# Performance work log

Hardware: AMD Instinct MI355X
Metric: run time of the kernel (lower is better)

## Reference

```python
import jax, jax.numpy as jnp
import numpy as np

ALPHA = 0.5
GAMMA = 0.01
TOP_K = 5
B, T, C = 2048, 8192, 1  # C must be 1 for amp_loss's grouped conv1d to be valid


def _ashift_loss(inp, tgt):
    _, t_len, _ = inp.shape
    sm = jax.nn.softmax(inp - tgt, axis=1)                      # [B,T,C]
    return jnp.mean(jnp.sum(jnp.abs(1.0 / t_len - sm), axis=1, keepdims=True))


def _phase_loss(inp, tgt, top_k=TOP_K):
    inp_f = jnp.fft.rfft(inp, axis=1)                           # [B,Tf,C] complex
    tgt_f = jnp.fft.rfft(tgt, axis=1)
    b, tf_len, c = tgt_f.shape
    amp = jnp.abs(tgt_f).at[:, 0, :].set(0.0)                   # zero DC bin
    # top-k magnitudes along freq axis (per batch, per channel)
    _, idx = jax.lax.top_k(jnp.transpose(amp, (0, 2, 1)), top_k)  # [B,C,k]
    top = jnp.transpose(idx, (0, 2, 1))                         # [B,k,C]
    # boolean mask: True everywhere except top-k freq bins (per column)
    freqs = jnp.arange(tf_len)
    mask = ~jnp.any(freqs[None, :, None, None] == top[:, None, :, :], axis=2)  # [B,Tf,C]
    # replicate torch row-major boolean-mask flatten + view(B, Tf-k, C):
    flat = mask.reshape(b, tf_len * c)
    order = jnp.argsort(~flat, axis=1, stable=True)             # kept (True) positions first, in row-major order
    keep = order[:, : (tf_len - top_k) * c]                     # flat (t*C + c') positions
    non_top = (keep // c).reshape(b, tf_len - top_k, c)         # stored value is the freq index t
    dom = jnp.take_along_axis(tgt_f, top, axis=1) - jnp.take_along_axis(inp_f, top, axis=1)
    domain_loss = jnp.mean(jnp.sqrt(jnp.sum(jnp.abs(dom) ** 2, axis=1)))
    gath = jnp.take_along_axis(inp_f, non_top, axis=1)          # [B,Tf-k,C]
    nondomain_loss = jnp.mean(jnp.sqrt(jnp.sum(jnp.abs(gath) ** 2, axis=1, keepdims=True)))
    return domain_loss + nondomain_loss


def _amp_loss(inp, tgt):
    # Valid only for C==1: conv1d([B,1,T], weight=[B,1,T], groups=1) -> [B,B,1]
    # out[b,o] = sum_t tgt[b,t] * flip(kernel)[o,t]
    t2 = tgt[:, :, 0]                                           # [B,T]
    i2 = inp[:, :, 0]
    flip_diff = t2[:, ::-1] - i2[:, ::-1]                       # flip(target) - flip(input)
    diff = jnp.einsum('bt,ot->bo', t2, flip_diff)               # self_corr - cross_corr, [B,B]
    # torch.norm(p=2) over the singleton dim == abs
    return jnp.mean(jnp.abs(diff))


def setup_inputs() -> dict:
    key = jax.random.key(0)
    k1, k2 = jax.random.split(key)
    inp = jax.random.normal(k1, (B, T, C), dtype=jnp.float32)
    tgt = jax.random.normal(k2, (B, T, C), dtype=jnp.float32)
    return {"input": inp, "target": tgt}


def reference(input, target):
    return (ALPHA * _ashift_loss(input, target)
            + (1.0 - ALPHA) * _phase_loss(input, target)
            + GAMMA * _amp_loss(input, target))
```

## Files before the change

### kernel.cpp

```cpp
#include <hip/hip_runtime.h>
#include <hip/hip_bf16.h>
#include <math.h>

#define B_N 2048
#define T_N 8192
#define NFFT 4096
#define TF_LEN 4097
#define TOPK 5
#define KSPLIT 4
#define GBK 64

#define ZIDX(n) ((n) + ((n) >> 4))
#define ZPAD (NFFT + (NFFT >> 4))

typedef float f32x4 __attribute__((ext_vector_type(4)));
typedef __bf16 bf16x8 __attribute__((ext_vector_type(8)));
typedef unsigned short ushort_t;

__device__ __forceinline__ void gload_lds16(const ushort_t* g, ushort_t* l) {
    __builtin_amdgcn_global_load_lds(
        (const __attribute__((address_space(1))) void*)g,
        (__attribute__((address_space(3))) void*)l,
        16, 0, 0);
}

__device__ __forceinline__ float wave_reduce_sum(float v) {
    for (int o = 32; o >= 1; o >>= 1) v += __shfl_xor(v, o, 64);
    return v;
}
__device__ __forceinline__ float wave_reduce_max(float v) {
    for (int o = 32; o >= 1; o >>= 1) v = fmaxf(v, __shfl_xor(v, o, 64));
    return v;
}

__device__ __forceinline__ ushort_t f2bf(float x) {
    __hip_bfloat16 h = __float2bfloat16(x);
    return *reinterpret_cast<ushort_t*>(&h);
}

__device__ __forceinline__ float2 cis_rev(float rev) {
    return make_float2(__builtin_amdgcn_cosf(rev), __builtin_amdgcn_sinf(rev));
}
__device__ __forceinline__ float2 cmulf(float2 a, float2 b) {
    return make_float2(a.x * b.x - a.y * b.y, a.x * b.y + a.y * b.x);
}

__global__ __launch_bounds__(256) void init_kernel(float* acc, float* Cpart, int nzbuf) {
    if (blockIdx.x == 0 && threadIdx.x < 4) acc[threadIdx.x] = 0.0f;
    if (nzbuf == 1) {
        size_t idx = ((size_t)blockIdx.x * 256 + threadIdx.x) * 4;
        *reinterpret_cast<f32x4*>(&Cpart[idx]) = (f32x4){0.f, 0.f, 0.f, 0.f};
    }
}

__device__ __forceinline__ void dft4(float2 x0, float2 x1, float2 x2, float2 x3,
                                     float2* y0, float2* y1, float2* y2, float2* y3) {
    float2 t0 = make_float2(x0.x + x2.x, x0.y + x2.y);
    float2 t1 = make_float2(x0.x - x2.x, x0.y - x2.y);
    float2 t2 = make_float2(x1.x + x3.x, x1.y + x3.y);
    float2 t3 = make_float2(x1.x - x3.x, x1.y - x3.y);
    *y0 = make_float2(t0.x + t2.x, t0.y + t2.y);
    *y2 = make_float2(t0.x - t2.x, t0.y - t2.y);
    *y1 = make_float2(t1.x + t3.y, t1.y - t3.x);
    *y3 = make_float2(t1.x - t3.y, t1.y + t3.x);
}

__device__ __forceinline__ void dft16(float2 X[16]) {
    float2 G[16];
    dft4(X[0], X[4], X[8],  X[12], &G[0],  &G[1],  &G[2],  &G[3]);
    dft4(X[1], X[5], X[9],  X[13], &G[4],  &G[5],  &G[6],  &G[7]);
    dft4(X[2], X[6], X[10], X[14], &G[8],  &G[9],  &G[10], &G[11]);
    dft4(X[3], X[7], X[11], X[15], &G[12], &G[13], &G[14], &G[15]);
    const float C1 = 0.9238795325112867f, S1 = 0.3826834323650898f;
    const float R2 = 0.7071067811865476f;
    G[5]  = cmulf(G[5],  make_float2(C1, -S1));
    G[6]  = cmulf(G[6],  make_float2(R2, -R2));
    G[7]  = cmulf(G[7],  make_float2(S1, -C1));
    G[9]  = cmulf(G[9],  make_float2(R2, -R2));
    { float2 g = G[10]; G[10] = make_float2(g.y, -g.x); }
    G[11] = cmulf(G[11], make_float2(-R2, -R2));
    G[13] = cmulf(G[13], make_float2(S1, -C1));
    G[14] = cmulf(G[14], make_float2(-R2, -R2));
    G[15] = cmulf(G[15], make_float2(-C1, S1));
    dft4(G[0], G[4], G[8],  G[12], &X[0], &X[4], &X[8],  &X[12]);
    dft4(G[1], G[5], G[9],  G[13], &X[1], &X[5], &X[9],  &X[13]);
    dft4(G[2], G[6], G[10], G[14], &X[2], &X[6], &X[10], &X[14]);
    dft4(G[3], G[7], G[11], G[15], &X[3], &X[7], &X[11], &X[15]);
}

__device__ __forceinline__ void rfft_bin(const float2* Zs, int k, float* orr, float* oi) {
    int kk = k & (NFFT - 1);
    int nk = (NFFT - k) & (NFFT - 1);
    float2 zk = Zs[ZIDX(kk)], znk = Zs[ZIDX(nk)];
    float xer = 0.5f * (zk.x + znk.x);
    float xei = 0.5f * (zk.y - znk.y);
    float xo_r = 0.5f * (zk.y + znk.y);
    float xo_i = -0.5f * (zk.x - znk.x);
    float2 w = cis_rev((float)k * (-1.0f / (float)T_N));
    *orr = xer + w.x * xo_r - w.y * xo_i;
    *oi = xei + w.x * xo_i + w.y * xo_r;
}

__global__ __launch_bounds__(256) void fused_row_kernel(const float* __restrict__ inp,
                                                        const float* __restrict__ tgt,
                                                        ushort_t* __restrict__ Abf,
                                                        ushort_t* __restrict__ Bbf,
                                                        float* acc) {
    __shared__ float2 Zs[ZPAD];
    __shared__ __align__(16) float amp[TF_LEN];
    __shared__ float red[4];
    __shared__ float wv[4];
    __shared__ int wi[4];
    __shared__ int topIdx[TOPK];
    __shared__ float2 tgtF[TOPK];
    __shared__ float rscratch[64];

    int b = blockIdx.x;
    int tid = threadIdx.x;
    int lane = tid & 63, wid = tid >> 6;
    const float* tp = tgt + (size_t)b * T_N;
    const float* ip = inp + (size_t)b * T_N;
    ushort_t* Ab = Abf + (size_t)b * T_N;
    ushort_t* Bb = Bbf + (size_t)b * T_N;

    float4 trv[8];
#pragma unroll
    for (int i = 0; i < 8; i++) {
        int q = tid + 256 * i;
        trv[i] = *reinterpret_cast<const float4*>(&tp[4 * q]);
        ushort4 ua;
        ua.x = f2bf(trv[i].x); ua.y = f2bf(trv[i].y);
        ua.z = f2bf(trv[i].z); ua.w = f2bf(trv[i].w);
        *reinterpret_cast<ushort4*>(&Ab[4 * q]) = ua;
        int m0 = 2 * q, m1 = 2 * q + 1;
        int p0 = ((m0 & 15) << 8) | (m0 & 0x0F0) | (m0 >> 8);
        int p1 = ((m1 & 15) << 8) | (m1 & 0x0F0) | (m1 >> 8);
        Zs[ZIDX(p0)] = make_float2(trv[i].x, trv[i].y);
        Zs[ZIDX(p1)] = make_float2(trv[i].z, trv[i].w);
    }

    float4 irv[8], dv[8];
#pragma unroll
    for (int i = 0; i < 8; i++) {
        int q = tid + 256 * i;
        irv[i] = *reinterpret_cast<const float4*>(&ip[4 * q]);
        dv[i] = make_float4(irv[i].x - trv[i].x, irv[i].y - trv[i].y,
                            irv[i].z - trv[i].z, irv[i].w - trv[i].w);
    }

    float* ampf = amp;
#pragma unroll
    for (int i = 0; i < 4; i++)
        *reinterpret_cast<float4*>(&ampf[4 * (tid + 256 * i)]) = dv[i];
    __syncthreads();
#pragma unroll
    for (int i2 = 0; i2 < 4; i2++) {
        int qr = 1024 + tid + 256 * i2;
        float4 v = *reinterpret_cast<const float4*>(&ampf[4 * (1023 - tid - 256 * i2)]);
        ushort4 ub;
        ub.x = f2bf(-v.w); ub.y = f2bf(-v.z); ub.z = f2bf(-v.y); ub.w = f2bf(-v.x);
        *reinterpret_cast<ushort4*>(&Bb[4 * qr]) = ub;
    }
    __syncthreads();
#pragma unroll
    for (int i = 4; i < 8; i++)
        *reinterpret_cast<float4*>(&ampf[4 * (tid + 256 * (i - 4))]) = dv[i];
    __syncthreads();
#pragma unroll
    for (int i2 = 0; i2 < 4; i2++) {
        int qr = tid + 256 * i2;
        float4 v = *reinterpret_cast<const float4*>(&ampf[4 * (1023 - tid - 256 * i2)]);
        ushort4 ub;
        ub.x = f2bf(-v.w); ub.y = f2bf(-v.z); ub.z = f2bf(-v.y); ub.w = f2bf(-v.x);
        *reinterpret_cast<ushort4*>(&Bb[4 * qr]) = ub;
    }
    __syncthreads();

    {
        float lmax = -1e30f;
#pragma unroll
        for (int i = 0; i < 8; i++)
            lmax = fmaxf(lmax, fmaxf(fmaxf(dv[i].x, dv[i].y), fmaxf(dv[i].z, dv[i].w)));
        lmax = wave_reduce_max(lmax);
        if (lane == 0) red[wid] = lmax;
        __syncthreads();
        float mx = fmaxf(fmaxf(red[0], red[1]), fmaxf(red[2], red[3]));
        __syncthreads();
        float lsum = 0.0f;
#pragma unroll
        for (int i = 0; i < 8; i++) {
            dv[i].x = __expf(dv[i].x - mx);
            dv[i].y = __expf(dv[i].y - mx);
            dv[i].z = __expf(dv[i].z - mx);
            dv[i].w = __expf(dv[i].w - mx);
            lsum += (dv[i].x + dv[i].y) + (dv[i].z + dv[i].w);
        }
        lsum = wave_reduce_sum(lsum);
        if (lane == 0) red[wid] = lsum;
        __syncthreads();
        float Z = (red[0] + red[1]) + (red[2] + red[3]);
        __syncthreads();
        float inv = 1.0f / Z;
        const float u = 1.0f / (float)T_N;
        float labs = 0.0f;
#pragma unroll
        for (int i = 0; i < 8; i++) {
            labs += fabsf(u - dv[i].x * inv) + fabsf(u - dv[i].y * inv) +
                    fabsf(u - dv[i].z * inv) + fabsf(u - dv[i].w * inv);
        }
        labs = wave_reduce_sum(labs);
        if (lane == 0) red[wid] = labs;
        __syncthreads();
        if (tid == 0)
            atomicAdd(acc + 0, (red[0] + red[1]) + (red[2] + red[3]));
    }
    __syncthreads();

    {
        float2 X[16];
        int base = tid * 16;
#pragma unroll
        for (int r = 0; r < 16; r++) X[r] = Zs[ZIDX(base + r)];
        dft16(X);
#pragma unroll
        for (int r = 0; r < 16; r++) Zs[ZIDX(base + r)] = X[r];
    }
    __syncthreads();
    {
        float2 X[16];
        int j = tid & 15;
        int base = (tid >> 4) * 256 + j;
#pragma unroll
        for (int r = 0; r < 16; r++) X[r] = Zs[ZIDX(base + 16 * r)];
        float2 w1 = cis_rev(-(float)j * (1.0f / 256.0f));
        float2 w = w1;
#pragma unroll
        for (int r = 1; r < 16; r++) { X[r] = cmulf(X[r], w); w = cmulf(w, w1); }
        dft16(X);
#pragma unroll
        for (int r = 0; r < 16; r++) Zs[ZIDX(base + 16 * r)] = X[r];
    }
    __syncthreads();
    {
        float2 X[16];
#pragma unroll
        for (int r = 0; r < 16; r++) X[r] = Zs[ZIDX(tid + 256 * r)];
        float2 w1 = cis_rev(-(float)tid * (1.0f / 4096.0f));
        float2 w = w1;
#pragma unroll
        for (int r = 1; r < 16; r++) { X[r] = cmulf(X[r], w); w = cmulf(w, w1); }
        dft16(X);
#pragma unroll
        for (int r = 0; r < 16; r++) Zs[ZIDX(tid + 256 * r)] = X[r];
    }
    __syncthreads();

    {
        float2 rot = cis_rev(-(float)tid * (1.0f / (float)T_N));
        const float2 drot = make_float2(0.9807852804032304f, -0.19509032201612825f);
#pragma unroll
        for (int i = 0; i < 16; i++) {
            int k = tid + 256 * i;
            if (k == 0) {
                amp[0] = -1.0f;
            } else {
                int nk = (NFFT - k) & (NFFT - 1);
                float2 zk = Zs[ZIDX(k & (NFFT - 1))], znk = Zs[ZIDX(nk)];
                float xer = 0.5f * (zk.x + znk.x);
                float xei = 0.5f * (zk.y - znk.y);
                float xo_r = 0.5f * (zk.y + znk.y);
                float xo_i = -0.5f * (zk.x - znk.x);
                float xr = xer + rot.x * xo_r - rot.y * xo_i;
                float xi = xei + rot.x * xo_i + rot.y * xo_r;
                amp[k] = xr * xr + xi * xi;
            }
            rot = cmulf(rot, drot);
        }
        if (tid == 0) {
            float2 z0 = Zs[ZIDX(0)];
            float v = z0.x - z0.y;
            amp[4096] = v * v;
        }
    }
    __syncthreads();

    for (int r = 0; r < TOPK; r++) {
        float bv = -3.0f;
        int bi = TF_LEN;
        for (int k = tid; k < TF_LEN; k += 256) {
            float a = amp[k];
            if (a > bv) { bv = a; bi = k; }
        }
        for (int o = 1; o < 64; o <<= 1) {
            float ov = __shfl_xor(bv, o, 64);
            int oi = __shfl_xor(bi, o, 64);
            if (ov > bv || (ov == bv && oi < bi)) { bv = ov; bi = oi; }
        }
        if (lane == 0) { wv[wid] = bv; wi[wid] = bi; }
        __syncthreads();
        if (tid == 0) {
            float fv = wv[0];
            int fi = wi[0];
            for (int w = 1; w < 4; w++)
                if (wv[w] > fv || (wv[w] == fv && wi[w] < fi)) { fv = wv[w]; fi = wi[w]; }
            topIdx[r] = fi;
            amp[fi] = -2.0f;
        }
        __syncthreads();
    }

    if (tid < TOPK) {
        float xr, xi;
        rfft_bin(Zs, topIdx[tid], &xr, &xi);
        tgtF[tid] = make_float2(xr, xi);
    }
    __syncthreads();

    int fq[TOPK];
#pragma unroll
    for (int q = 0; q < TOPK; q++) fq[q] = topIdx[q];

    float2 cur[TOPK], wc[TOPK], wf[TOPK];
    float re[TOPK], im[TOPK];
#pragma unroll
    for (int q = 0; q < TOPK; q++) {
        int f = fq[q];
        cur[q] = cis_rev(-(float)((f * 4 * tid) & (T_N - 1)) * (1.0f / (float)T_N));
        wc[q] = cis_rev(-(float)f * (1.0f / (float)T_N));
        wf[q] = cis_rev(-(float)((f * 1021) & (T_N - 1)) * (1.0f / (float)T_N));
        re[q] = 0.0f; im[q] = 0.0f;
    }
    float E = 0.0f, sev = 0.0f, sod = 0.0f;
#pragma unroll
    for (int i = 0; i < 8; i++) {
        float vv0 = irv[i].x, vv1 = irv[i].y, vv2 = irv[i].z, vv3 = irv[i].w;
        E = fmaf(vv0, vv0, E); sev += vv0;
#pragma unroll
        for (int q = 0; q < TOPK; q++) {
            re[q] = fmaf(vv0, cur[q].x, re[q]); im[q] = fmaf(vv0, cur[q].y, im[q]);
            cur[q] = cmulf(cur[q], wc[q]);
        }
        E = fmaf(vv1, vv1, E); sod += vv1;
#pragma unroll
        for (int q = 0; q < TOPK; q++) {
            re[q] = fmaf(vv1, cur[q].x, re[q]); im[q] = fmaf(vv1, cur[q].y, im[q]);
            cur[q] = cmulf(cur[q], wc[q]);
        }
        E = fmaf(vv2, vv2, E); sev += vv2;
#pragma unroll
        for (int q = 0; q < TOPK; q++) {
            re[q] = fmaf(vv2, cur[q].x, re[q]); im[q] = fmaf(vv2, cur[q].y, im[q]);
            cur[q] = cmulf(cur[q], wc[q]);
        }
        E = fmaf(vv3, vv3, E); sod += vv3;
#pragma unroll
        for (int q = 0; q < TOPK; q++) {
            re[q] = fmaf(vv3, cur[q].x, re[q]); im[q] = fmaf(vv3, cur[q].y, im[q]);
            cur[q] = cmulf(cur[q], wf[q]);
        }
    }

    float vals[13] = {re[0], im[0], re[1], im[1], re[2], im[2], re[3], im[3],
                      re[4], im[4], E, sev + sod, sev - sod};
#pragma unroll
    for (int i = 0; i < 13; i++) {
        float v = wave_reduce_sum(vals[i]);
        if (lane == 0) rscratch[wid * 13 + i] = v;
    }
    __syncthreads();
    if (tid == 0) {
        float tot[13];
        for (int i = 0; i < 13; i++)
            tot[i] = rscratch[i] + rscratch[13 + i] + rscratch[26 + i] + rscratch[39 + i];
        float dsum = 0, isum = 0;
        for (int q = 0; q < TOPK; q++) {
            float rr = tot[2 * q], ii = tot[2 * q + 1];
            float dr = tgtF[q].x - rr, di = tgtF[q].y - ii;
            dsum += dr * dr + di * di;
            isum += rr * rr + ii * ii;
        }
        float Ee = tot[10], X0v = tot[11], Xhv = tot[12];
        float S_all = 0.5f * ((float)T_N * Ee + X0v * X0v + Xhv * Xhv);
        float val = sqrtf(dsum) + sqrtf(fmaxf(S_all - isum, 0.0f));
        atomicAdd(acc + 1, val);
    }
}

__global__ __launch_bounds__(512, 2) void gemm_kernel(const ushort_t* __restrict__ A,
                                                      const ushort_t* __restrict__ Bm,
                                                      float* __restrict__ Cpart,
                                                      int nzbuf) {
    __shared__ __align__(16) ushort_t lds[2][4][128 * 64];
    int tid = threadIdx.x;
    int bid = blockIdx.x;
    int swz = ((bid & 7) << 5) | (bid >> 3);
    int bx = swz & 7, by = (swz >> 3) & 7, bz = swz >> 6;
    int row0 = bx * 256, col0 = by * 256;
    const int KC = T_N / KSPLIT;
    const int NT = KC / GBK;
    const int NIT = NT / 2;
    int kbase = bz * KC;

    int w = tid >> 6, lane = tid & 63;
    int wm = w >> 2, wn = w & 3;
    int lr = lane & 15, kq = lane >> 4;

    f32x4 accf[8][4];
#pragma unroll
    for (int mi = 0; mi < 8; mi++)
#pragma unroll
        for (int ni = 0; ni < 4; ni++) accf[mi][ni] = (f32x4){0.f, 0.f, 0.f, 0.f};

    int strow = tid >> 3;
    int scb = (tid & 7) ^ (strow & 7);
    const ushort_t* gA0 = A + (size_t)(row0 + strow) * T_N + kbase + scb * 8;
    const ushort_t* gA1 = A + (size_t)(row0 + 128 + strow) * T_N + kbase + scb * 8;
    const ushort_t* gB0 = Bm + (size_t)(col0 + strow) * T_N + kbase + scb * 8;
    const ushort_t* gB1 = Bm + (size_t)(col0 + 128 + strow) * T_N + kbase + scb * 8;
    const size_t SUB = (size_t)64 * T_N;

    int rb0 = lr * 64 + ((kq ^ (lr & 7)) << 3);
    int rb1 = lr * 64 + (((4 + kq) ^ (lr & 7)) << 3);

#define SA_(s, buf, kt)                                                        \
    do {                                                                       \
        gload_lds16(gA0 + (s) * SUB + (size_t)(kt) * GBK, &lds[buf][0][(s) * 4096 + tid * 8]); \
        gload_lds16(gA1 + (s) * SUB + (size_t)(kt) * GBK, &lds[buf][1][(s) * 4096 + tid * 8]); \
    } while (0)
#define SB_(rg, buf, kt)                                                       \
    do {                                                                       \
        const ushort_t* g_ = ((rg) == 2) ? gB0 : gB1;                          \
        gload_lds16(g_ + (size_t)(kt) * GBK, &lds[buf][rg][tid * 8]);          \
        gload_lds16(g_ + SUB + (size_t)(kt) * GBK, &lds[buf][rg][4096 + tid * 8]); \
    } while (0)

#define PHASE(BUF, QM, QN, VMN, STAGE_STMT)                                    \
    do {                                                                       \
        asm volatile("s_waitcnt vmcnt(" #VMN ")" ::: "memory");                \
        const ushort_t* Ab_ = &lds[BUF][wm][0];                                \
        const ushort_t* Bb_ = &lds[BUF][2 + (wn >> 1)][(wn & 1) * 4096];       \
        bf16x8 a_[4][2], b_[2][2];                                             \
        _Pragma("unroll") for (int m_ = 0; m_ < 4; m_++) {                     \
            a_[m_][0] = *reinterpret_cast<const bf16x8*>(Ab_ + (QM) * 4096 + m_ * 1024 + rb0); \
            a_[m_][1] = *reinterpret_cast<const bf16x8*>(Ab_ + (QM) * 4096 + m_ * 1024 + rb1); \
        }                                                                      \
        _Pragma("unroll") for (int n_ = 0; n_ < 2; n_++) {                     \
            b_[n_][0] = *reinterpret_cast<const bf16x8*>(Bb_ + (QN) * 2048 + n_ * 1024 + rb0); \
            b_[n_][1] = *reinterpret_cast<const bf16x8*>(Bb_ + (QN) * 2048 + n_ * 1024 + rb1); \
        }                                                                      \
        STAGE_STMT;                                                            \
        __builtin_amdgcn_s_barrier();                                          \
        __builtin_amdgcn_s_setprio(1);                                         \
        _Pragma("unroll") for (int m_ = 0; m_ < 4; m_++)                       \
        _Pragma("unroll") for (int n_ = 0; n_ < 2; n_++) {                     \
            accf[(QM) * 4 + m_][(QN) * 2 + n_] = __builtin_amdgcn_mfma_f32_16x16x32_bf16( \
                a_[m_][0], b_[n_][0], accf[(QM) * 4 + m_][(QN) * 2 + n_], 0, 0, 0); \
            accf[(QM) * 4 + m_][(QN) * 2 + n_] = __builtin_amdgcn_mfma_f32_16x16x32_bf16( \
                a_[m_][1], b_[n_][1], accf[(QM) * 4 + m_][(QN) * 2 + n_], 0, 0, 0); \
        }                                                                      \
        __builtin_amdgcn_s_setprio(0);                                         \
        __builtin_amdgcn_s_barrier();                                          \
    } while (0)

    SA_(0, 0, 0);
    SA_(1, 0, 0);
    SB_(2, 0, 0);
    SB_(3, 0, 0);
    SA_(0, 1, 1);
    asm volatile("s_waitcnt vmcnt(2)" ::: "memory");
    __builtin_amdgcn_s_barrier();

    for (int it = 0; it < NIT; ++it) {
        int kt1 = 2 * it + 1;
        int te = (2 * it + 2 < NT) ? 2 * it + 2 : 2 * it;
        int to = (kt1 + 2 < NT) ? kt1 + 2 : kt1;
        PHASE(0, 0, 0, 4, SB_(3, 1, kt1));
        PHASE(0, 0, 1, 4, SB_(2, 1, kt1));
        PHASE(0, 1, 0, 6, SA_(0, 0, te));
        PHASE(0, 1, 1, 2, SA_(1, 1, kt1));
        PHASE(1, 0, 0, 4, SB_(3, 0, te));
        PHASE(1, 0, 1, 2, SB_(2, 0, te));
        PHASE(1, 1, 0, 4, SA_(1, 0, te));
        PHASE(1, 1, 1, 2, SA_(0, 1, to));
    }
#undef PHASE
#undef SA_
#undef SB_

    int crow = row0 + wm * 128 + (lane >> 4) * 4;
    int ccol = col0 + wn * 64 + lr;
    if (nzbuf == 4) {
        float* Cp = Cpart + (size_t)bz * ((size_t)B_N * B_N);
#pragma unroll
        for (int mi = 0; mi < 8; mi++)
#pragma unroll
            for (int ni = 0; ni < 4; ni++)
#pragma unroll
                for (int r = 0; r < 4; r++)
                    Cp[(size_t)(crow + mi * 16 + r) * B_N + ccol + ni * 16] =
                        accf[mi][ni][r];
    } else {
#pragma unroll
        for (int mi = 0; mi < 8; mi++)
#pragma unroll
            for (int ni = 0; ni < 4; ni++)
#pragma unroll
                for (int r = 0; r < 4; r++)
                    atomicAdd(&Cpart[(size_t)(crow + mi * 16 + r) * B_N + ccol + ni * 16],
                              accf[mi][ni][r]);
    }
}

__global__ __launch_bounds__(256) void absum_kernel(const float* __restrict__ C,
                                                    float* acc, int nzbuf) {
    __shared__ float sred[4];
    int tid = threadIdx.x;
    int lane = tid & 63, wid = tid >> 6;
    const size_t NN = (size_t)B_N * B_N;
    size_t base = (size_t)blockIdx.x * 4096;
    float s = 0.0f;
#pragma unroll
    for (int i = 0; i < 4; i++) {
        size_t idx = base + (size_t)(tid + 256 * i) * 4;
        f32x4 v = *reinterpret_cast<const f32x4*>(&C[idx]);
        if (nzbuf == 4) {
            v += *reinterpret_cast<const f32x4*>(&C[NN + idx]);
            v += *reinterpret_cast<const f32x4*>(&C[2 * NN + idx]);
            v += *reinterpret_cast<const f32x4*>(&C[3 * NN + idx]);
        }
        s += fabsf(v.x) + fabsf(v.y) + fabsf(v.z) + fabsf(v.w);
    }
    s = wave_reduce_sum(s);
    if (lane == 0) sred[wid] = s;
    __syncthreads();
    if (tid == 0) atomicAdd(acc + 2, sred[0] + sred[1] + sred[2] + sred[3]);
}

__global__ void combine_kernel(const float* acc, float* out) {
    if (threadIdx.x == 0) {
        float ash = acc[0] / (float)B_N;
        float ph = acc[1] / (float)B_N;
        float am = acc[2] / ((float)B_N * (float)B_N);
        out[0] = 0.5f * ash + 0.5f * ph + 0.01f * am;
    }
}

extern "C" void kernel_launch(void* const* d_in, const int* in_sizes, int n_in,
                              void* d_out, int out_size, void* d_ws, size_t ws_size,
                              hipStream_t stream) {
    const float* inp = (const float*)d_in[0];
    const float* tgt = (const float*)d_in[1];
    float* acc = (float*)d_ws;
    ushort_t* Abf = (ushort_t*)((char*)d_ws + 256);
    ushort_t* Bbf = Abf + (size_t)B_N * T_N;
    float* Cpart = (float*)(Bbf + (size_t)B_N * T_N);
    float* out = (float*)d_out;

    size_t need4 = 256 + 2 * (size_t)B_N * T_N * sizeof(ushort_t)
                 + (size_t)KSPLIT * (size_t)B_N * B_N * sizeof(float);
    int nzbuf = (ws_size >= need4) ? 4 : 1;

    hipLaunchKernelGGL(init_kernel, dim3(nzbuf == 1 ? 4096 : 1), dim3(256), 0, stream,
                       acc, Cpart, nzbuf);
    hipLaunchKernelGGL(fused_row_kernel, dim3(B_N), dim3(256), 0, stream,
                       inp, tgt, Abf, Bbf, acc);
    hipLaunchKernelGGL(gemm_kernel, dim3(256), dim3(512), 0, stream,
                       Abf, Bbf, Cpart, nzbuf);
    hipLaunchKernelGGL(absum_kernel, dim3(1024), dim3(256), 0, stream,
                       Cpart, acc, nzbuf);
    hipLaunchKernelGGL(combine_kernel, dim3(1), dim3(1), 0, stream, acc, out);
}
```

Baseline: 184.0 us.

## Keep FFT magnitudes in registers and drop LDS amp buffer for reversal

```diff
diff --git a/kernel.cpp b/kernel.cpp
--- a/kernel.cpp
+++ b/kernel.cpp
@@ -101,13 +101,12 @@
     *oi = xei + w.x * xo_i + w.y * xo_r;
 }
 
-__global__ __launch_bounds__(256) void fused_row_kernel(const float* __restrict__ inp,
-                                                        const float* __restrict__ tgt,
-                                                        ushort_t* __restrict__ Abf,
-                                                        ushort_t* __restrict__ Bbf,
-                                                        float* acc) {
+__global__ __launch_bounds__(256, 4) void fused_row_kernel(const float* __restrict__ inp,
+                                                           const float* __restrict__ tgt,
+                                                           ushort_t* __restrict__ Abf,
+                                                           ushort_t* __restrict__ Bbf,
+                                                           float* acc) {
     __shared__ float2 Zs[ZPAD];
-    __shared__ __align__(16) float amp[TF_LEN];
     __shared__ float red[4];
     __shared__ float wv[4];
     __shared__ int wi[4];
@@ -146,35 +145,11 @@
         irv[i] = *reinterpret_cast<const float4*>(&ip[4 * q]);
         dv[i] = make_float4(irv[i].x - trv[i].x, irv[i].y - trv[i].y,
                             irv[i].z - trv[i].z, irv[i].w - trv[i].w);
-    }
-
-    float* ampf = amp;
-#pragma unroll
-    for (int i = 0; i < 4; i++)
-        *reinterpret_cast<float4*>(&ampf[4 * (tid + 256 * i)]) = dv[i];
-    __syncthreads();
-#pragma unroll
-    for (int i2 = 0; i2 < 4; i2++) {
-        int qr = 1024 + tid + 256 * i2;
-        float4 v = *reinterpret_cast<const float4*>(&ampf[4 * (1023 - tid - 256 * i2)]);
         ushort4 ub;
-        ub.x = f2bf(-v.w); ub.y = f2bf(-v.z); ub.z = f2bf(-v.y); ub.w = f2bf(-v.x);
-        *reinterpret_cast<ushort4*>(&Bb[4 * qr]) = ub;
-    }
-    __syncthreads();
-#pragma unroll
-    for (int i = 4; i < 8; i++)
-        *reinterpret_cast<float4*>(&ampf[4 * (tid + 256 * (i - 4))]) = dv[i];
-    __syncthreads();
-#pragma unroll
-    for (int i2 = 0; i2 < 4; i2++) {
-        int qr = tid + 256 * i2;
-        float4 v = *reinterpret_cast<const float4*>(&ampf[4 * (1023 - tid - 256 * i2)]);
-        ushort4 ub;
-        ub.x = f2bf(-v.w); ub.y = f2bf(-v.z); ub.z = f2bf(-v.y); ub.w = f2bf(-v.x);
-        *reinterpret_cast<ushort4*>(&Bb[4 * qr]) = ub;
-    }
-    __syncthreads();
+        ub.x = f2bf(-dv[i].w); ub.y = f2bf(-dv[i].z);
+        ub.z = f2bf(-dv[i].y); ub.w = f2bf(-dv[i].x);
+        *reinterpret_cast<ushort4*>(&Bb[4 * (2047 - q)]) = ub;
+    }
 
     {
         float lmax = -1e30f;
@@ -255,14 +230,16 @@
     }
     __syncthreads();
 
+    float av[16];
+    float aN = -3.0f;
     {
         float2 rot = cis_rev(-(float)tid * (1.0f / (float)T_N));
         const float2 drot = make_float2(0.9807852804032304f, -0.19509032201612825f);
 #pragma unroll
         for (int i = 0; i < 16; i++) {
             int k = tid + 256 * i;
-            if (k == 0) {
-                amp[0] = -1.0f;
+            if (i == 0 && tid == 0) {
+                av[i] = -1.0f;
             } else {
                 int nk = (NFFT - k) & (NFFT - 1);
                 float2 zk = Zs[ZIDX(k & (NFFT - 1))], znk = Zs[ZIDX(nk)];
@@ -272,25 +249,26 @@
                 float xo_i = -0.5f * (zk.x - znk.x);
                 float xr = xer + rot.x * xo_r - rot.y * xo_i;
                 float xi = xei + rot.x * xo_i + rot.y * xo_r;
-                amp[k] = xr * xr + xi * xi;
+                av[i] = xr * xr + xi * xi;
             }
             rot = cmulf(rot, drot);
         }
         if (tid == 0) {
             float2 z0 = Zs[ZIDX(0)];
             float v = z0.x - z0.y;
-            amp[4096] = v * v;
-        }
-    }
-    __syncthreads();
+            aN = v * v;
+        }
+    }
 
     for (int r = 0; r < TOPK; r++) {
         float bv = -3.0f;
         int bi = TF_LEN;
-        for (int k = tid; k < TF_LEN; k += 256) {
-            float a = amp[k];
-            if (a > bv) { bv = a; bi = k; }
-        }
+#pragma unroll
+        for (int i = 0; i < 16; i++) {
+            float a = av[i];
+            if (a > bv) { bv = a; bi = tid + 256 * i; }
+        }
+        if (aN > bv) { bv = aN; bi = 4096; }
         for (int o = 1; o < 64; o <<= 1) {
             float ov = __shfl_xor(bv, o, 64);
             int oi = __shfl_xor(bi, o, 64);
@@ -304,9 +282,17 @@
             for (int w = 1; w < 4; w++)
                 if (wv[w] > fv || (wv[w] == fv && wi[w] < fi)) { fv = wv[w]; fi = wi[w]; }
             topIdx[r] = fi;
-            amp[fi] = -2.0f;
-        }
-        __syncthreads();
+        }
+        __syncthreads();
+        int fi = topIdx[r];
+        if (fi == 4096) {
+            if (tid == 0) aN = -2.0f;
+        } else if ((fi & 255) == tid) {
+            int slot = fi >> 8;
+#pragma unroll
+            for (int i = 0; i < 16; i++)
+                if (i == slot) av[i] = -2.0f;
+        }
     }
 
     if (tid < TOPK) {
```

Result: slower. 189.7 us (+3.1%).
